# Optimization experiments

Measured on AMD Instinct MI355X. Metric: run time of the kernel, lower is better.

## Reference

```python
import jax, jax.numpy as jnp
import numpy as np

B, C_EDGE, C_FUSED, C_SEM = 4, 64, 128, 128
H = W = 64
MASK_SIZE = 11
EPS = 1e-6


def _window_mask(h, w, mask_size):
    # M_dw: 0 inside the clipped (mask_size x mask_size) window around each query pixel, -10000 outside.
    half = mask_size // 2
    idx = jnp.arange(h * w)
    qx, qy = idx // w, idx % w
    inside = (jnp.abs(qx[:, None] - qx[None, :]) <= half) & (jnp.abs(qy[:, None] - qy[None, :]) <= half)
    return jnp.where(inside, 0.0, -10000.0).astype(jnp.float32)


def _conv1x1(x, w, b):
    # x: [b, cin, h, w], w: [cout, cin]
    return jnp.einsum('bchw,oc->bohw', x, w) + b[None, :, None, None]


def _proj1d(x, w, b):
    # x: [b, cin, n], w: [cout, cin]
    return jnp.einsum('bcn,oc->bon', x, w) + b[None, :, None]


def _bilinear(x, h, w):
    # matches F.interpolate(mode='bilinear', align_corners=False)
    b, c = x.shape[0], x.shape[1]
    return jax.image.resize(x, (b, c, h, w), method='linear', antialias=False)


def setup_inputs() -> dict:
    key = jax.random.key(0)
    ks = jax.random.split(key, 13)
    s = 0.05
    return {
        'edge_features': jax.random.normal(ks[0], (B, C_EDGE, 32, 32), jnp.float32),
        'semantic_features': jax.random.normal(ks[1], (B, C_SEM, H, W), jnp.float32),
        'fused_features': jax.random.normal(ks[2], (B, C_FUSED, 32, 32), jnp.float32),
        'w_align': jax.random.normal(ks[3], (C_SEM, C_EDGE), jnp.float32) * s,
        'b_align': jax.random.normal(ks[4], (C_SEM,), jnp.float32) * s,
        'w_fused_align': jax.random.normal(ks[5], (C_SEM, C_FUSED), jnp.float32) * s,
        'b_fused_align': jax.random.normal(ks[6], (C_SEM,), jnp.float32) * s,
        'w_q': jax.random.normal(ks[7], (2 * C_SEM, 2 * C_SEM), jnp.float32) * s,
        'b_q': jax.random.normal(ks[8], (2 * C_SEM,), jnp.float32) * s,
        'w_k': jax.random.normal(ks[9], (2 * C_SEM, 2 * C_SEM), jnp.float32) * s,
        'b_k': jax.random.normal(ks[10], (2 * C_SEM,), jnp.float32) * s,
        'w_fusion': jax.random.normal(ks[11], (C_SEM, 2 * C_SEM), jnp.float32) * s,
        'b_fusion': jax.random.normal(ks[12], (C_SEM,), jnp.float32) * s,
    }


def reference(edge_features, semantic_features, fused_features,
              w_align, b_align, w_fused_align, b_fused_align,
              w_q, b_q, w_k, b_k, w_fusion, b_fusion):
    b, c, h, w = semantic_features.shape
    n = h * w

    edge = _conv1x1(_bilinear(edge_features, h, w), w_align, b_align)            # [b,c,h,w]
    fused = _conv1x1(_bilinear(fused_features, h, w), w_fused_align, b_fused_align)

    l2_edge = jnp.sqrt(jnp.sum(edge * edge, axis=1, keepdims=True))              # [b,1,h,w]
    l2_sem = jnp.sqrt(jnp.sum(semantic_features * semantic_features, axis=1, keepdims=True))
    similarity = jnp.sum((edge / (l2_edge + EPS)) * (semantic_features / (l2_sem + EPS)),
                         axis=1, keepdims=True)
    similarity = (similarity + 1.0) * 0.5

    density_flat = l2_edge.reshape(b, n)
    density = (jax.nn.softmax(density_flat, axis=1) * n).reshape(b, 1, h, w)

    edge_t = (edge * similarity).reshape(b, c, n)
    sem_t = (semantic_features * density).reshape(b, c, n)
    fused_t = fused.reshape(b, c, n)
    sem_raw = semantic_features.reshape(b, c, n)

    edge_cat = jnp.concatenate([edge_t, edge_t], axis=1)    # [b,2c,n]
    sem_cat = jnp.concatenate([sem_t, fused_t], axis=1)
    sem_val = jnp.concatenate([sem_raw, fused_t], axis=1)

    q = _proj1d(edge_cat, w_q, b_q)                          # [b,2c,n]
    k = _proj1d(sem_cat, w_k, b_k)

    scale = 1.0 / jnp.sqrt(jnp.float32(2 * c))
    attn = jnp.einsum('bcn,bcm->bnm', q, k) * scale          # [b,n,n]
    attn = attn + _window_mask(h, w, MASK_SIZE)
    attn = jax.nn.softmax(attn, axis=-1)

    out = jnp.einsum('bnm,bcm->bnc', attn, sem_val)          # [b,n,2c]
    out = out.reshape(b, h, w, 2 * c).transpose(0, 3, 1, 2)  # [b,2c,h,w]
    return _conv1x1(out, w_fusion, b_fusion)
```

## Files before the change

### kernel.cpp

```cpp
#include <hip/hip_runtime.h>
#include <hip/hip_bf16.h>

#define NB 4
#define C 128
#define N 4096
#define EPS 1e-6f
#define PW 80
#define PIMG 5120

typedef float f32x4 __attribute__((ext_vector_type(4)));
typedef short bf16x8 __attribute__((ext_vector_type(8)));
typedef unsigned short ushort_t;
typedef unsigned int uint_t;

__device__ __forceinline__ ushort_t f2bf(float f) {
  __hip_bfloat16 h = __float2bfloat16(f);
  return *reinterpret_cast<ushort_t*>(&h);
}

struct alignas(8) us4 { ushort_t a, b, c, d; };

__device__ __forceinline__ void conv_body(const float* __restrict__ x,
                                          const float* __restrict__ w,
                                          const float* __restrict__ bias,
                                          float* __restrict__ out,
                                          int n0, int o0, int b, int CIN) {
  const float* xb = x + (size_t)(b * CIN) * 1024 + n0;
  float ax0 = 0.f, ay0 = 0.f, ax1 = 0.f, ay1 = 0.f;
  float ax2 = 0.f, ay2 = 0.f, ax3 = 0.f, ay3 = 0.f;
#pragma unroll 4
  for (int c = 0; c < CIN; ++c) {
    float2 xv = *(const float2*)(xb + (size_t)c * 1024);
    float w0 = w[(o0 + 0) * CIN + c];
    float w1 = w[(o0 + 1) * CIN + c];
    float w2 = w[(o0 + 2) * CIN + c];
    float w3 = w[(o0 + 3) * CIN + c];
    ax0 += w0 * xv.x; ay0 += w0 * xv.y;
    ax1 += w1 * xv.x; ay1 += w1 * xv.y;
    ax2 += w2 * xv.x; ay2 += w2 * xv.y;
    ax3 += w3 * xv.x; ay3 += w3 * xv.y;
  }
  size_t ob = ((size_t)b * 128 + o0) * 1024 + n0;
  float b0 = bias[o0], b1 = bias[o0 + 1], b2 = bias[o0 + 2], b3 = bias[o0 + 3];
  *(float2*)(out + ob)        = make_float2(ax0 + b0, ay0 + b0);
  *(float2*)(out + ob + 1024) = make_float2(ax1 + b1, ay1 + b1);
  *(float2*)(out + ob + 2048) = make_float2(ax2 + b2, ay2 + b2);
  *(float2*)(out + ob + 3072) = make_float2(ax3 + b3, ay3 + b3);
}

__global__ void prep_misc(const float* __restrict__ edge_f, const float* __restrict__ w_align,
                          const float* __restrict__ b_align,
                          const float* __restrict__ fused_f, const float* __restrict__ w_fal,
                          const float* __restrict__ b_fal,
                          const float* __restrict__ wq, const float* __restrict__ wk,
                          const float* __restrict__ wf,
                          ushort_t* __restrict__ wqf, ushort_t* __restrict__ wkf,
                          ushort_t* __restrict__ wff,
                          float* __restrict__ edge32, float* __restrict__ fused32,
                          float* __restrict__ dsum) {
  int bx = blockIdx.x, t = threadIdx.x;
  if (bx < 64) {
    if (bx == 0 && t < NB) dsum[t] = 0.f;
    int c = bx * 256 + t;
    int lane = c & 63;
    int mrow = lane & 15, quad = lane >> 4;
    if (c < 4096) {
      int grp = c >> 6;
      int tile = grp >> 2, kslot = grp & 3;
      int o = tile * 16 + mrow, k0 = kslot * 32 + quad * 8;
      const float* s = wq + o * 256 + k0;
      ushort_t* d = wqf + (size_t)c * 8;
#pragma unroll
      for (int j = 0; j < 8; ++j) d[j] = f2bf(s[j] + s[128 + j]);
    } else if (c < 12288) {
      int c2 = c - 4096;
      int grp = c2 >> 6;
      int tile = grp >> 3, kslot = grp & 7;
      int o = tile * 16 + mrow, k0 = kslot * 32 + quad * 8;
      const float* s = wk + o * 256 + k0;
      ushort_t* d = wkf + (size_t)c2 * 8;
#pragma unroll
      for (int j = 0; j < 8; ++j) d[j] = f2bf(s[j]);
    } else {
      int c2 = c - 12288;
      int grp = c2 >> 6;
      int tile = grp >> 3, kslot = grp & 7;
      int o = tile * 16 + mrow, k0 = kslot * 32 + quad * 8;
      const float* s = wf + o * 256 + k0;
      ushort_t* d = wff + (size_t)c2 * 8;
#pragma unroll
      for (int j = 0; j < 8; ++j) d[j] = f2bf(s[j]);
    }
  } else if (bx < 320) {
    int j = bx - 64;
    int b = j >> 6, rem = j & 63;
    int og = rem >> 1, half = rem & 1;
    conv_body(edge_f, w_align, b_align, edge32, half * 512 + t * 2, og * 4, b, 64);
  } else {
    int j = bx - 320;
    int b = j >> 6, rem = j & 63;
    int og = rem >> 1, half = rem & 1;
    conv_body(fused_f, w_fal, b_fal, fused32, half * 512 + t * 2, og * 4, b, 128);
  }
}

__global__ __launch_bounds__(512, 4) void prep_acts(const float* __restrict__ edge32,
                                                    const float* __restrict__ fused32,
                                                    const float* __restrict__ sem,
                                                    const ushort_t* __restrict__ wqf,
                                                    const ushort_t* __restrict__ wff,
                                                    const float* __restrict__ b_q,
                                                    ushort_t* __restrict__ xt_sem,
                                                    ushort_t* __restrict__ xt_fused,
                                                    float* __restrict__ simb,
                                                    float* __restrict__ l2e,
                                                    float* __restrict__ dsum,
                                                    ushort_t* __restrict__ qtb,
                                                    ushort_t* __restrict__ v2b) {
  int b = blockIdx.y, bx = blockIdx.x;
  int y = bx >> 1, xh = (bx & 1) * 32;
  int t = threadIdx.x;
  int nl = t & 31, cg = t >> 5;
  int x = xh + nl;
  int yy0 = (y & 1) ? (y >> 1) : (y >> 1) - 1;
  float fy = (y & 1) ? 0.25f : 0.75f;
  int y0c = max(yy0, 0), y1c = min(yy0 + 1, 31);
  int xx0 = (x & 1) ? (x >> 1) : (x >> 1) - 1;
  float fx = (x & 1) ? 0.25f : 0.75f;
  int x0c = max(xx0, 0), x1c = min(xx0 + 1, 31);

  __shared__ uint_t se[32][68], ssm[32][68], sf[32][68];
  __shared__ float red[8][3][32];
  __shared__ float simL[32];
  __shared__ ushort_t vstg[128 * 40];

  float ee = 0.f, ssum = 0.f, es = 0.f;
#pragma unroll
  for (int p = 0; p < 4; ++p) {
    float evs[2], fvs[2], svs[2];
#pragma unroll
    for (int u = 0; u < 2; ++u) {
      int c = cg * 8 + p * 2 + u;
      const float* ip = edge32 + ((size_t)(b * 128 + c)) * 1024;
      float e00 = ip[y0c * 32 + x0c], e01 = ip[y0c * 32 + x1c];
      float e10 = ip[y1c * 32 + x0c], e11 = ip[y1c * 32 + x1c];
      float ev = (1.f - fy) * ((1.f - fx) * e00 + fx * e01) + fy * ((1.f - fx) * e10 + fx * e11);
      const float* fp = fused32 + ((size_t)(b * 128 + c)) * 1024;
      float f00 = fp[y0c * 32 + x0c], f01 = fp[y0c * 32 + x1c];
      float f10 = fp[y1c * 32 + x0c], f11 = fp[y1c * 32 + x1c];
      float fv = (1.f - fy) * ((1.f - fx) * f00 + fx * f01) + fy * ((1.f - fx) * f10 + fx * f11);
      float sv = sem[((size_t)(b * 128 + c)) * 4096 + y * 64 + x];
      ee += ev * ev; ssum += sv * sv; es += ev * sv;
      evs[u] = ev; fvs[u] = fv; svs[u] = sv;
    }
    int col = cg * 4 + p;
    se[nl][col]  = (uint_t)f2bf(evs[0]) | ((uint_t)f2bf(evs[1]) << 16);
    sf[nl][col]  = (uint_t)f2bf(fvs[0]) | ((uint_t)f2bf(fvs[1]) << 16);
    ssm[nl][col] = (uint_t)f2bf(svs[0]) | ((uint_t)f2bf(svs[1]) << 16);
  }
  ee += __shfl_xor(ee, 32, 64); ssum += __shfl_xor(ssum, 32, 64); es += __shfl_xor(es, 32, 64);
  int w = t >> 6, lane = t & 63;
  int l15 = lane & 15, quad = lane >> 4;
  if (lane < 32) { red[w][0][lane] = ee; red[w][1][lane] = ssum; red[w][2][lane] = es; }
  __syncthreads();

  int base_n = b * 4096 + y * 64 + xh;
#pragma unroll
  for (int rep = 0; rep < 4; ++rep) {
    int d = rep * 512 + t;
    int r = d >> 6, cp = d & 63;
    ((uint_t*)xt_sem)[(size_t)(base_n + r) * 64 + cp] = ssm[r][cp];
    ((uint_t*)xt_fused)[(size_t)(base_n + r) * 64 + cp] = sf[r][cp];
  }
  if (t < 32) {
    float E = 0.f, S = 0.f, X = 0.f;
#pragma unroll
    for (int w2 = 0; w2 < 8; ++w2) { E += red[w2][0][t]; S += red[w2][1][t]; X += red[w2][2][t]; }
    float le = sqrtf(E), ls = sqrtf(S);
    float sv = (X / ((le + EPS) * (ls + EPS)) + 1.f) * 0.5f;
    simb[base_n + t] = sv;
    simL[t] = sv;
    l2e[base_n + t] = le;
    float pe = expf(le - 16.f);
#pragma unroll
    for (int m2 = 16; m2; m2 >>= 1) pe += __shfl_xor(pe, m2, 64);
    if (t == 0) atomicAdd(&dsum[b], pe);
  }
  __syncthreads();

#pragma unroll
  for (int h = 0; h < 2; ++h) {
    f32x4 vacc = (f32x4){0.f,0.f,0.f,0.f};
#pragma unroll
    for (int kk = 0; kk < 4; ++kk) {
      bf16x8 bfr = *(const bf16x8*)&ssm[h * 16 + l15][kk * 16 + quad * 4];
      bf16x8 afr = *(const bf16x8*)(wff + (size_t)((w * 8 + kk) * 64 + lane) * 8);
      vacc = __builtin_amdgcn_mfma_f32_16x16x32_bf16(afr, bfr, vacc, 0, 0, 0);
    }
#pragma unroll
    for (int kk = 0; kk < 4; ++kk) {
      bf16x8 bfr = *(const bf16x8*)&sf[h * 16 + l15][kk * 16 + quad * 4];
      bf16x8 afr = *(const bf16x8*)(wff + (size_t)((w * 8 + 4 + kk) * 64 + lane) * 8);
      vacc = __builtin_amdgcn_mfma_f32_16x16x32_bf16(afr, bfr, vacc, 0, 0, 0);
    }
#pragma unroll
    for (int r = 0; r < 4; ++r) {
      int ch = w * 16 + quad * 4 + r;
      vstg[ch * 40 + h * 16 + l15] = f2bf(vacc[r]);
    }
  }

#pragma unroll
  for (int h = 0; h < 2; ++h) {
    f32x4 qacc[2];
#pragma unroll
    for (int i = 0; i < 2; ++i) qacc[i] = (f32x4){0.f,0.f,0.f,0.f};
#pragma unroll
    for (int kk = 0; kk < 4; ++kk) {
      bf16x8 bfr = *(const bf16x8*)&se[h * 16 + l15][kk * 16 + quad * 4];
#pragma unroll
      for (int i = 0; i < 2; ++i) {
        bf16x8 afr = *(const bf16x8*)(wqf + (size_t)(((w * 2 + i) * 4 + kk) * 64 + lane) * 8);
        qacc[i] = __builtin_amdgcn_mfma_f32_16x16x32_bf16(afr, bfr, qacc[i], 0, 0, 0);
      }
    }
    int px = h * 16 + l15;
    float sv = simL[px];
    int n = y * 64 + xh + px;
#pragma unroll
    for (int i = 0; i < 2; ++i) {
      int o = (w * 2 + i) * 16 + quad * 4;
      float4 bq = *(const float4*)(b_q + o);
      us4 pk = { f2bf(sv * qacc[i][0] + bq.x), f2bf(sv * qacc[i][1] + bq.y),
                 f2bf(sv * qacc[i][2] + bq.z), f2bf(sv * qacc[i][3] + bq.w) };
      *(us4*)(qtb + ((size_t)b * N + n) * 256 + o) = pk;
    }
  }

  __syncthreads();
  int np0 = y * PW + 8 + xh;
  {
    int ch = t >> 2, seg = t & 3;
    *(bf16x8*)(v2b + ((size_t)b * 128 + ch) * PIMG + np0 + seg * 8) =
        *(const bf16x8*)&vstg[ch * 40 + seg * 8];
  }
}

__global__ __launch_bounds__(256, 4) void gemm_k(const ushort_t* __restrict__ xt_sem,
                                                 const ushort_t* __restrict__ xt_fused,
                                                 const ushort_t* __restrict__ wkf,
                                                 const float* __restrict__ b_k,
                                                 const float* __restrict__ l2e,
                                                 const float* __restrict__ dsum,
                                                 ushort_t* __restrict__ ktb) {
  int bx = blockIdx.x, bI = blockIdx.y;
  int t = threadIdx.x, w = t >> 6, lane = t & 63;
  int mrow = lane & 15, quad = lane >> 4;
  __shared__ __align__(16) ushort_t stg[16 * 264];

  int n0 = bx * 16, o0 = w * 64;
  float dscale = 4096.f / dsum[bI];
  const ushort_t* bS = xt_sem + ((size_t)bI * N + n0 + mrow) * 128 + quad * 8;
  const ushort_t* bF = xt_fused + ((size_t)bI * N + n0 + mrow) * 128 + quad * 8;
  f32x4 accL[4], accR[4];
#pragma unroll
  for (int i = 0; i < 4; ++i) { accL[i] = (f32x4){0.f,0.f,0.f,0.f}; accR[i] = (f32x4){0.f,0.f,0.f,0.f}; }
#pragma unroll
  for (int kk = 0; kk < 4; ++kk) {
    bf16x8 bfr = *(const bf16x8*)(bS + kk * 32);
#pragma unroll
    for (int i = 0; i < 4; ++i) {
      bf16x8 afr = *(const bf16x8*)(wkf + (size_t)((((w * 4 + i) * 8) + kk) * 64 + lane) * 8);
      accL[i] = __builtin_amdgcn_mfma_f32_16x16x32_bf16(afr, bfr, accL[i], 0, 0, 0);
    }
  }
#pragma unroll
  for (int kk = 0; kk < 4; ++kk) {
    bf16x8 bfr = *(const bf16x8*)(bF + kk * 32);
#pragma unroll
    for (int i = 0; i < 4; ++i) {
      bf16x8 afr = *(const bf16x8*)(wkf + (size_t)((((w * 4 + i) * 8) + 4 + kk) * 64 + lane) * 8);
      accR[i] = __builtin_amdgcn_mfma_f32_16x16x32_bf16(afr, bfr, accR[i], 0, 0, 0);
    }
  }
  int n = n0 + mrow;
  float dv = expf(l2e[bI * N + n] - 16.f) * dscale;
#pragma unroll
  for (int i = 0; i < 4; ++i) {
    int o = o0 + i * 16 + quad * 4;
    float4 bk = *(const float4*)(b_k + o);
    us4 pk = { f2bf(accL[i][0] * dv + accR[i][0] + bk.x),
               f2bf(accL[i][1] * dv + accR[i][1] + bk.y),
               f2bf(accL[i][2] * dv + accR[i][2] + bk.z),
               f2bf(accL[i][3] * dv + accR[i][3] + bk.w) };
    *(us4*)&stg[mrow * 264 + o] = pk;
  }
  __syncthreads();
  int np0 = (n0 >> 6) * PW + 8 + (n0 & 63);
#pragma unroll
  for (int r = 0; r < 2; ++r) {
    int cidx = r * 256 + t;
    int row = cidx >> 5, cc = cidx & 31;
    *(bf16x8*)(ktb + ((size_t)bI * PIMG + np0 + row) * 256 + cc * 8) =
        *(const bf16x8*)&stg[row * 264 + cc * 8];
  }
}

__global__ __launch_bounds__(256) void attn_kernel(const ushort_t* __restrict__ qtb,
                                                   const ushort_t* __restrict__ ktb,
                                                   const ushort_t* __restrict__ v2b,
                                                   const float* __restrict__ b_fusion,
                                                   float* __restrict__ out) {
  int L = blockIdx.x;
  int xcd = L & 7, j = L >> 3;
  int b = xcd >> 1;
  int ty0 = (((xcd & 1) << 3) + (j >> 3)) * 4;
  int tx0 = (j & 7) * 8;
  int y0 = max(ty0 - 5, 0), y1 = min(ty0 + 8, 63);
  int nh = y1 - y0 + 1;
  int x0a = tx0 - 8, cb = tx0;
  int ntq = (nh * 3 + 1) >> 1;
  int npv = (nh * 3 + 3) >> 2;

  __shared__ ushort_t pst[32][352];
  __shared__ float redm[4][2][16], reds[4][2][16];

  int t = threadIdx.x, w = t >> 6, lane = t & 63;
  int l15 = lane & 15, quad = lane >> 4;

  int gap = npv * 32 - ntq * 16;
  for (int idx = t; idx < 32 * gap; idx += 256)
    pst[idx & 31][ntq * 16 + (idx >> 5)] = 0;

  int n_s0 = (ty0 + (l15 >> 3)) * 64 + tx0 + (l15 & 7);
  int n_s1 = n_s0 + 128;
  bf16x8 qfr[2][8];
  {
    const ushort_t* q0 = qtb + ((size_t)b * N + n_s0) * 256 + quad * 8;
    const ushort_t* q1 = qtb + ((size_t)b * N + n_s1) * 256 + quad * 8;
#pragma unroll
    for (int ks = 0; ks < 8; ++ks) {
      qfr[0][ks] = *(const bf16x8*)(q0 + ks * 32);
      qfr[1][ks] = *(const bf16x8*)(q1 + ks * 32);
    }
  }
  int qx = tx0 + (l15 & 7);
  int qy0 = ty0 + (l15 >> 3);

  const ushort_t* kb = ktb + (size_t)b * PIMG * 256;
  f32x4 sc[6][2];
#pragma unroll
  for (int i = 0; i < 6; ++i) {
    int tq = w + i * 4;
    if (tq >= ntq) break;
    int key = tq * 16 + l15;
    int ry = (key * 2731) >> 16;
    int rx = key - ry * 24;
    int yy = min(y0 + ry, 63);
    const ushort_t* krow = kb + (size_t)(yy * PW + cb + rx) * 256 + quad * 8;
    f32x4 a0 = (f32x4){0.f,0.f,0.f,0.f}, a1 = (f32x4){0.f,0.f,0.f,0.f};
#pragma unroll
    for (int ks = 0; ks < 8; ++ks) {
      bf16x8 afr = *(const bf16x8*)(krow + ks * 32);
      a0 = __builtin_amdgcn_mfma_f32_16x16x32_bf16(afr, qfr[0][ks], a0, 0, 0, 0);
      a1 = __builtin_amdgcn_mfma_f32_16x16x32_bf16(afr, qfr[1][ks], a1, 0, 0, 0);
    }
    sc[i][0] = a0; sc[i][1] = a1;
  }
  float mymax0 = -1e30f, mymax1 = -1e30f;
#pragma unroll
  for (int i = 0; i < 6; ++i) {
    int tq = w + i * 4;
    if (tq >= ntq) break;
#pragma unroll
    for (int r = 0; r < 4; ++r) {
      int key = tq * 16 + quad * 4 + r;
      int ry = (key * 2731) >> 16;
      int rx = key - ry * 24;
      int x = x0a + rx;
      int dx = x - qx;
      bool xok = (dx >= -5) && (dx <= 5) && (x >= 0) && (x <= 63) && (ry < nh);
      int dy0 = y0 + ry - qy0;
      float s0 = (xok && dy0 >= -5 && dy0 <= 5) ? sc[i][0][r] * 0.0625f : -1e30f;
      int dy1 = dy0 - 2;
      float s1 = (xok && dy1 >= -5 && dy1 <= 5) ? sc[i][1][r] * 0.0625f : -1e30f;
      sc[i][0][r] = s0; sc[i][1][r] = s1;
      mymax0 = fmaxf(mymax0, s0); mymax1 = fmaxf(mymax1, s1);
    }
  }
  mymax0 = fmaxf(mymax0, __shfl_xor(mymax0, 16, 64));
  mymax0 = fmaxf(mymax0, __shfl_xor(mymax0, 32, 64));
  mymax1 = fmaxf(mymax1, __shfl_xor(mymax1, 16, 64));
  mymax1 = fmaxf(mymax1, __shfl_xor(mymax1, 32, 64));
  if (quad == 0) { redm[w][0][l15] = mymax0; redm[w][1][l15] = mymax1; }
  __syncthreads();
  float gmax0 = fmaxf(fmaxf(redm[0][0][l15], redm[1][0][l15]), fmaxf(redm[2][0][l15], redm[3][0][l15]));
  float gmax1 = fmaxf(fmaxf(redm[0][1][l15], redm[1][1][l15]), fmaxf(redm[2][1][l15], redm[3][1][l15]));
  float mysum0 = 0.f, mysum1 = 0.f;
#pragma unroll
  for (int i = 0; i < 6; ++i) {
    int tq = w + i * 4;
    if (tq >= ntq) break;
#pragma unroll
    for (int r = 0; r < 4; ++r) {
      float e0 = expf(sc[i][0][r] - gmax0);
      float e1 = expf(sc[i][1][r] - gmax1);
      sc[i][0][r] = e0; sc[i][1][r] = e1;
      mysum0 += e0; mysum1 += e1;
    }
  }
  mysum0 += __shfl_xor(mysum0, 16, 64); mysum0 += __shfl_xor(mysum0, 32, 64);
  mysum1 += __shfl_xor(mysum1, 16, 64); mysum1 += __shfl_xor(mysum1, 32, 64);
  if (quad == 0) { reds[w][0][l15] = mysum0; reds[w][1][l15] = mysum1; }
#pragma unroll
  for (int i = 0; i < 6; ++i) {
    int tq = w + i * 4;
    if (tq >= ntq) break;
    int kc = tq * 16 + quad * 4;
#pragma unroll
    for (int s = 0; s < 2; ++s) {
      uint_t p01 = (uint_t)f2bf(sc[i][s][0]) | ((uint_t)f2bf(sc[i][s][1]) << 16);
      uint_t p23 = (uint_t)f2bf(sc[i][s][2]) | ((uint_t)f2bf(sc[i][s][3]) << 16);
      *(uint_t*)(&pst[s * 16 + l15][kc]) = p01;
      *(uint_t*)(&pst[s * 16 + l15][kc + 2]) = p23;
    }
  }
  __syncthreads();

  float rinv0 = 1.f / (reds[0][0][l15] + reds[1][0][l15] + reds[2][0][l15] + reds[3][0][l15]);
  float rinv1 = 1.f / (reds[0][1][l15] + reds[1][1][l15] + reds[2][1][l15] + reds[3][1][l15]);

  const ushort_t* vb = v2b + (size_t)b * 128 * PIMG;
#pragma unroll
  for (int half = 0; half < 2; ++half) {
    int ch0 = half * 64 + w * 16;
    const ushort_t* vrow = vb + (size_t)(ch0 + l15) * PIMG;
    f32x4 acc0 = (f32x4){0.f,0.f,0.f,0.f}, acc1 = (f32x4){0.f,0.f,0.f,0.f};
    for (int ks = 0; ks < npv; ++ks) {
      int kst = ks * 32 + quad * 8;
      int ry = (kst * 2731) >> 16;
      int rxs = kst - ry * 24;
      int yy = min(y0 + ry, 63);
      bf16x8 av = *(const bf16x8*)(vrow + yy * PW + cb + rxs);
      bf16x8 bp0 = *(const bf16x8*)(&pst[l15][kst]);
      bf16x8 bp1 = *(const bf16x8*)(&pst[16 + l15][kst]);
      acc0 = __builtin_amdgcn_mfma_f32_16x16x32_bf16(av, bp0, acc0, 0, 0, 0);
      acc1 = __builtin_amdgcn_mfma_f32_16x16x32_bf16(av, bp1, acc1, 0, 0, 0);
    }
    int chg = ch0 + quad * 4;
    float4 bf4 = *(const float4*)(b_fusion + chg);
    float bfa[4] = {bf4.x, bf4.y, bf4.z, bf4.w};
#pragma unroll
    for (int r = 0; r < 4; ++r) {
      out[((size_t)b * 128 + chg + r) * N + n_s0] = acc0[r] * rinv0 + bfa[r];
      out[((size_t)b * 128 + chg + r) * N + n_s1] = acc1[r] * rinv1 + bfa[r];
    }
  }
}

extern "C" void kernel_launch(void* const* d_in, const int* in_sizes, int n_in,
                              void* d_out, int out_size, void* d_ws, size_t ws_size,
                              hipStream_t stream) {
  (void)in_sizes; (void)n_in; (void)out_size; (void)ws_size;
  const float* edge_f  = (const float*)d_in[0];
  const float* sem     = (const float*)d_in[1];
  const float* fused_f = (const float*)d_in[2];
  const float* w_align = (const float*)d_in[3];
  const float* b_align = (const float*)d_in[4];
  const float* w_fal   = (const float*)d_in[5];
  const float* b_fal   = (const float*)d_in[6];
  const float* w_q     = (const float*)d_in[7];
  const float* b_q     = (const float*)d_in[8];
  const float* w_k     = (const float*)d_in[9];
  const float* b_k     = (const float*)d_in[10];
  const float* w_fus   = (const float*)d_in[11];
  const float* b_fus   = (const float*)d_in[12];
  float* out = (float*)d_out;

  float* ws = (float*)d_ws;
  float* edge32   = ws;
  float* fused32  = ws + 524288;
  float* simb     = ws + 1048576;
  float* l2e      = ws + 1064960;
  float* dsum     = ws + 1081344;
  ushort_t* xt_sem   = (ushort_t*)(ws + 1097728);
  ushort_t* xt_fused = (ushort_t*)(ws + 2146304);
  ushort_t* wqf      = (ushort_t*)(ws + 3194880);
  ushort_t* wkf      = (ushort_t*)(ws + 3211264);
  ushort_t* wff      = (ushort_t*)(ws + 3244032);
  ushort_t* qtb      = (ushort_t*)(ws + 3260416);
  ushort_t* ktb      = (ushort_t*)(ws + 5357568);
  ushort_t* v2b      = (ushort_t*)(ws + 7979008);

  prep_misc<<<576, 256, 0, stream>>>(edge_f, w_align, b_align, fused_f, w_fal, b_fal,
                                     w_q, w_k, w_fus, wqf, wkf, wff, edge32, fused32, dsum);
  prep_acts<<<dim3(128, NB), 512, 0, stream>>>(edge32, fused32, sem, wqf, wff, b_q,
                                               xt_sem, xt_fused, simb, l2e, dsum, qtb, v2b);
  gemm_k<<<dim3(256, NB), 256, 0, stream>>>(xt_sem, xt_fused, wkf, b_k, l2e, dsum, ktb);
  attn_kernel<<<512, 256, 0, stream>>>(qtb, ktb, v2b, b_fus, out);
}
```

Measured before the change: 157.3 us.

## Fuse K projection into prep_acts and split density sum into small kernel

```diff
diff --git a/kernel.cpp b/kernel.cpp
--- a/kernel.cpp
+++ b/kernel.cpp
@@ -104,18 +104,61 @@
   }
 }
 
+__global__ __launch_bounds__(512) void l2ek(const float* __restrict__ edge32,
+                                            float* __restrict__ dsum) {
+  int b = blockIdx.y, bx = blockIdx.x;
+  int y = bx >> 1, xh = (bx & 1) * 32;
+  int t = threadIdx.x;
+  int nl = t & 31, cg = t >> 5;
+  int x = xh + nl;
+  int yy0 = (y & 1) ? (y >> 1) : (y >> 1) - 1;
+  float fy = (y & 1) ? 0.25f : 0.75f;
+  int y0c = max(yy0, 0), y1c = min(yy0 + 1, 31);
+  int xx0 = (x & 1) ? (x >> 1) : (x >> 1) - 1;
+  float fx = (x & 1) ? 0.25f : 0.75f;
+  int x0c = max(xx0, 0), x1c = min(xx0 + 1, 31);
+
+  __shared__ float red[8][32];
+  float ee = 0.f;
+#pragma unroll
+  for (int p = 0; p < 4; ++p) {
+#pragma unroll
+    for (int u = 0; u < 2; ++u) {
+      int c = cg * 8 + p * 2 + u;
+      const float* ip = edge32 + ((size_t)(b * 128 + c)) * 1024;
+      float e00 = ip[y0c * 32 + x0c], e01 = ip[y0c * 32 + x1c];
+      float e10 = ip[y1c * 32 + x0c], e11 = ip[y1c * 32 + x1c];
+      float ev = (1.f - fy) * ((1.f - fx) * e00 + fx * e01) + fy * ((1.f - fx) * e10 + fx * e11);
+      ee += ev * ev;
+    }
+  }
+  ee += __shfl_xor(ee, 32, 64);
+  int w = t >> 6, lane = t & 63;
+  if (lane < 32) red[w][lane] = ee;
+  __syncthreads();
+  if (t < 32) {
+    float E = 0.f;
+#pragma unroll
+    for (int w2 = 0; w2 < 8; ++w2) E += red[w2][t];
+    float le = sqrtf(E);
+    float pe = expf(le - 16.f);
+#pragma unroll
+    for (int m2 = 16; m2; m2 >>= 1) pe += __shfl_xor(pe, m2, 64);
+    if (t == 0) atomicAdd(&dsum[b], pe);
+  }
+}
+
 __global__ __launch_bounds__(512, 4) void prep_acts(const float* __restrict__ edge32,
                                                     const float* __restrict__ fused32,
                                                     const float* __restrict__ sem,
                                                     const ushort_t* __restrict__ wqf,
+                                                    const ushort_t* __restrict__ wkf,
                                                     const ushort_t* __restrict__ wff,
                                                     const float* __restrict__ b_q,
-                                                    ushort_t* __restrict__ xt_sem,
-                                                    ushort_t* __restrict__ xt_fused,
-                                                    float* __restrict__ simb,
-                                                    float* __restrict__ l2e,
-                                                    float* __restrict__ dsum,
+                                                    const float* __restrict__ b_k,
+                                                    const float* __restrict__ dsum,
                                                     ushort_t* __restrict__ qtb,
+                                                    ushort_t* __restrict__ ktb,
                                                     ushort_t* __restrict__ v2b) {
   int b = blockIdx.y, bx = blockIdx.x;
   int y = bx >> 1, xh = (bx & 1) * 32;
@@ -131,8 +174,11 @@
 
   __shared__ uint_t se[32][68], ssm[32][68], sf[32][68];
   __shared__ float red[8][3][32];
-  __shared__ float simL[32];
+  __shared__ float simL[32], l2eL[32];
   __shared__ ushort_t vstg[128 * 40];
+  __shared__ __align__(16) ushort_t kstg[32 * 264];
+
+  float dscale = 4096.f / dsum[b];
 
   float ee = 0.f, ssum = 0.f, es = 0.f;
 #pragma unroll
@@ -164,29 +210,18 @@
   if (lane < 32) { red[w][0][lane] = ee; red[w][1][lane] = ssum; red[w][2][lane] = es; }
   __syncthreads();
 
-  int base_n = b * 4096 + y * 64 + xh;
-#pragma unroll
-  for (int rep = 0; rep < 4; ++rep) {
-    int d = rep * 512 + t;
-    int r = d >> 6, cp = d & 63;
-    ((uint_t*)xt_sem)[(size_t)(base_n + r) * 64 + cp] = ssm[r][cp];
-    ((uint_t*)xt_fused)[(size_t)(base_n + r) * 64 + cp] = sf[r][cp];
-  }
   if (t < 32) {
     float E = 0.f, S = 0.f, X = 0.f;
 #pragma unroll
     for (int w2 = 0; w2 < 8; ++w2) { E += red[w2][0][t]; S += red[w2][1][t]; X += red[w2][2][t]; }
     float le = sqrtf(E), ls = sqrtf(S);
     float sv = (X / ((le + EPS) * (ls + EPS)) + 1.f) * 0.5f;
-    simb[base_n + t] = sv;
     simL[t] = sv;
-    l2e[base_n + t] = le;
-    float pe = expf(le - 16.f);
-#pragma unroll
-    for (int m2 = 16; m2; m2 >>= 1) pe += __shfl_xor(pe, m2, 64);
-    if (t == 0) atomicAdd(&dsum[b], pe);
+    l2eL[t] = le;
   }
   __syncthreads();
+
+  int np0 = y * PW + 8 + xh;
 
 #pragma unroll
   for (int h = 0; h < 2; ++h) {
@@ -207,6 +242,42 @@
     for (int r = 0; r < 4; ++r) {
       int ch = w * 16 + quad * 4 + r;
       vstg[ch * 40 + h * 16 + l15] = f2bf(vacc[r]);
+    }
+  }
+
+#pragma unroll
+  for (int h = 0; h < 2; ++h) {
+    f32x4 aL[2], aR[2];
+#pragma unroll
+    for (int i = 0; i < 2; ++i) { aL[i] = (f32x4){0.f,0.f,0.f,0.f}; aR[i] = (f32x4){0.f,0.f,0.f,0.f}; }
+#pragma unroll
+    for (int kk = 0; kk < 4; ++kk) {
+      bf16x8 bfr = *(const bf16x8*)&ssm[h * 16 + l15][kk * 16 + quad * 4];
+#pragma unroll
+      for (int i = 0; i < 2; ++i) {
+        bf16x8 afr = *(const bf16x8*)(wkf + (size_t)((((w * 2 + i) * 8) + kk) * 64 + lane) * 8);
+        aL[i] = __builtin_amdgcn_mfma_f32_16x16x32_bf16(afr, bfr, aL[i], 0, 0, 0);
+      }
+    }
+#pragma unroll
+    for (int kk = 0; kk < 4; ++kk) {
+      bf16x8 bfr = *(const bf16x8*)&sf[h * 16 + l15][kk * 16 + quad * 4];
+#pragma unroll
+      for (int i = 0; i < 2; ++i) {
+        bf16x8 afr = *(const bf16x8*)(wkf + (size_t)((((w * 2 + i) * 8) + 4 + kk) * 64 + lane) * 8);
+        aR[i] = __builtin_amdgcn_mfma_f32_16x16x32_bf16(afr, bfr, aR[i], 0, 0, 0);
+      }
+    }
+    float dv = expf(l2eL[h * 16 + l15] - 16.f) * dscale;
+#pragma unroll
+    for (int i = 0; i < 2; ++i) {
+      int o = (w * 2 + i) * 16 + quad * 4;
+      float4 bk4 = *(const float4*)(b_k + o);
+      us4 pk = { f2bf(aL[i][0] * dv + aR[i][0] + bk4.x),
+                 f2bf(aL[i][1] * dv + aR[i][1] + bk4.y),
+                 f2bf(aL[i][2] * dv + aR[i][2] + bk4.z),
+                 f2bf(aL[i][3] * dv + aR[i][3] + bk4.w) };
+      *(us4*)&kstg[(h * 16 + l15) * 264 + o] = pk;
     }
   }
 
@@ -238,71 +309,17 @@
   }
 
   __syncthreads();
-  int np0 = y * PW + 8 + xh;
   {
     int ch = t >> 2, seg = t & 3;
     *(bf16x8*)(v2b + ((size_t)b * 128 + ch) * PIMG + np0 + seg * 8) =
         *(const bf16x8*)&vstg[ch * 40 + seg * 8];
   }
-}
-
-__global__ __launch_bounds__(256, 4) void gemm_k(const ushort_t* __restrict__ xt_sem,
-                                                 const ushort_t* __restrict__ xt_fused,
-                                                 const ushort_t* __restrict__ wkf,
-                                                 const float* __restrict__ b_k,
-                                                 const float* __restrict__ l2e,
-                                                 const float* __restrict__ dsum,
-                                                 ushort_t* __restrict__ ktb) {
-  int bx = blockIdx.x, bI = blockIdx.y;
-  int t = threadIdx.x, w = t >> 6, lane = t & 63;
-  int mrow = lane & 15, quad = lane >> 4;
-  __shared__ __align__(16) ushort_t stg[16 * 264];
-
-  int n0 = bx * 16, o0 = w * 64;
-  float dscale = 4096.f / dsum[bI];
-  const ushort_t* bS = xt_sem + ((size_t)bI * N + n0 + mrow) * 128 + quad * 8;
-  const ushort_t* bF = xt_fused + ((size_t)bI * N + n0 + mrow) * 128 + quad * 8;
-  f32x4 accL[4], accR[4];
-#pragma unroll
-  for (int i = 0; i < 4; ++i) { accL[i] = (f32x4){0.f,0.f,0.f,0.f}; accR[i] = (f32x4){0.f,0.f,0.f,0.f}; }
-#pragma unroll
-  for (int kk = 0; kk < 4; ++kk) {
-    bf16x8 bfr = *(const bf16x8*)(bS + kk * 32);
-#pragma unroll
-    for (int i = 0; i < 4; ++i) {
-      bf16x8 afr = *(const bf16x8*)(wkf + (size_t)((((w * 4 + i) * 8) + kk) * 64 + lane) * 8);
-      accL[i] = __builtin_amdgcn_mfma_f32_16x16x32_bf16(afr, bfr, accL[i], 0, 0, 0);
-    }
-  }
-#pragma unroll
-  for (int kk = 0; kk < 4; ++kk) {
-    bf16x8 bfr = *(const bf16x8*)(bF + kk * 32);
-#pragma unroll
-    for (int i = 0; i < 4; ++i) {
-      bf16x8 afr = *(const bf16x8*)(wkf + (size_t)((((w * 4 + i) * 8) + 4 + kk) * 64 + lane) * 8);
-      accR[i] = __builtin_amdgcn_mfma_f32_16x16x32_bf16(afr, bfr, accR[i], 0, 0, 0);
-    }
-  }
-  int n = n0 + mrow;
-  float dv = expf(l2e[bI * N + n] - 16.f) * dscale;
-#pragma unroll
-  for (int i = 0; i < 4; ++i) {
-    int o = o0 + i * 16 + quad * 4;
-    float4 bk = *(const float4*)(b_k + o);
-    us4 pk = { f2bf(accL[i][0] * dv + accR[i][0] + bk.x),
-               f2bf(accL[i][1] * dv + accR[i][1] + bk.y),
-               f2bf(accL[i][2] * dv + accR[i][2] + bk.z),
-               f2bf(accL[i][3] * dv + accR[i][3] + bk.w) };
-    *(us4*)&stg[mrow * 264 + o] = pk;
-  }
-  __syncthreads();
-  int np0 = (n0 >> 6) * PW + 8 + (n0 & 63);
 #pragma unroll
   for (int r = 0; r < 2; ++r) {
-    int cidx = r * 256 + t;
-    int row = cidx >> 5, cc = cidx & 31;
-    *(bf16x8*)(ktb + ((size_t)bI * PIMG + np0 + row) * 256 + cc * 8) =
-        *(const bf16x8*)&stg[row * 264 + cc * 8];
+    int idx = r * 512 + t;
+    int row = idx >> 5, cc = idx & 31;
+    *(bf16x8*)(ktb + ((size_t)b * PIMG + np0 + row) * 256 + cc * 8) =
+        *(const bf16x8*)&kstg[row * 264 + cc * 8];
   }
 }
 
@@ -480,11 +497,7 @@
   float* ws = (float*)d_ws;
   float* edge32   = ws;
   float* fused32  = ws + 524288;
-  float* simb     = ws + 1048576;
-  float* l2e      = ws + 1064960;
   float* dsum     = ws + 1081344;
-  ushort_t* xt_sem   = (ushort_t*)(ws + 1097728);
-  ushort_t* xt_fused = (ushort_t*)(ws + 2146304);
   ushort_t* wqf      = (ushort_t*)(ws + 3194880);
   ushort_t* wkf      = (ushort_t*)(ws + 3211264);
   ushort_t* wff      = (ushort_t*)(ws + 3244032);
@@ -494,8 +507,8 @@
 
   prep_misc<<<576, 256, 0, stream>>>(edge_f, w_align, b_align, fused_f, w_fal, b_fal,
                                      w_q, w_k, w_fus, wqf, wkf, wff, edge32, fused32, dsum);
-  prep_acts<<<dim3(128, NB), 512, 0, stream>>>(edge32, fused32, sem, wqf, wff, b_q,
-                                               xt_sem, xt_fused, simb, l2e, dsum, qtb, v2b);
-  gemm_k<<<dim3(256, NB), 256, 0, stream>>>(xt_sem, xt_fused, wkf, b_k, l2e, dsum, ktb);
+  l2ek<<<dim3(128, NB), 512, 0, stream>>>(edge32, dsum);
+  prep_acts<<<dim3(128, NB), 512, 0, stream>>>(edge32, fused32, sem, wqf, wkf, wff,
+                                               b_q, b_k, dsum, qtb, ktb, v2b);
   attn_kernel<<<512, 256, 0, stream>>>(qtb, ktb, v2b, b_fus, out);
 }
```

New measurement: 164.6 us. +4.7%, slower.
